# Kernel tuning notes

Hardware: AMD Instinct MI355X
Metric: run time of the kernel (lower is better)

## Reference

```python
import jax, jax.numpy as jnp
import numpy as np

B, H, W = 8, 64, 64
D = 256          # in_dim == key_dim == value_dim
HEADS = 8
DK = D // HEADS  # per-head channels (key == value)
EPS = 1e-5


def _ln(x, g, b):
    m = jnp.mean(x, axis=-1, keepdims=True)
    v = jnp.var(x, axis=-1, keepdims=True)
    return (x - m) * jax.lax.rsqrt(v + EPS) * g + b


def setup_inputs() -> dict:
    key = jax.random.key(0)
    ks = jax.random.split(key, 8)
    return {
        "x1": jax.random.normal(ks[0], (B, H, W, 2 * D), jnp.float32),
        "x2": jax.random.normal(ks[1], (B, H, W, D), jnp.float32),
        "linear_w": jax.random.normal(ks[2], (2 * D, D), jnp.float32) * 0.02,
        "linear_b": jax.random.normal(ks[3], (D,), jnp.float32) * 0.02,
        "ln1_g": jnp.ones((D,), jnp.float32) + jax.random.normal(ks[4], (D,), jnp.float32) * 0.02,
        "ln1_b": jax.random.normal(ks[5], (D,), jnp.float32) * 0.02,
        "reproj_w": jax.random.normal(ks[6], (2 * D, D), jnp.float32) * 0.02,  # 1x1 conv kernel [out,in]
        "reproj_b": jax.random.normal(ks[7], (2 * D,), jnp.float32) * 0.02,
        "ln_attn_g": jnp.ones((2 * D,), jnp.float32),
        "ln_attn_b": jnp.zeros((2 * D,), jnp.float32),
    }


def _cross_attention(n1, n2, reproj_w, reproj_b, ln_g, ln_b):
    # n1 (values source), n2 (keys/queries source): [B,H,W,D]
    N = H * W
    v = n1.reshape(B, N, D).transpose(0, 2, 1).reshape(B, HEADS, DK, N)
    kq = n2.reshape(B, N, D).transpose(0, 2, 1).reshape(B, HEADS, DK, N)
    k = jax.nn.softmax(kq, axis=-1)  # softmax over tokens (dim=2 in torch slice)
    q = jax.nn.softmax(kq, axis=2)   # softmax over per-head channels (dim=1 in torch slice)
    # attended[b,h,d,n] = sum_m sum_e q[b,h,d,m] k[b,h,e,m] v[b,h,e,n]
    ctx = jnp.einsum('bhdm,bhem->bhde', q, k)          # [B,h,dk,dk]
    att = jnp.einsum('bhde,bhen->bhdn', ctx, v)        # [B,h,dk,N]
    agg = att.reshape(B, D, H, W)                      # concat heads along channels
    rep = jnp.einsum('od,bdhw->bohw', reproj_w, agg) + reproj_b[None, :, None, None]
    rep = rep.transpose(0, 2, 3, 1)                    # [B,H,W,2D]
    return _ln(rep, ln_g, ln_b)


def reference(x1, x2, linear_w, linear_b, ln1_g, ln1_b, reproj_w, reproj_b, ln_attn_g, ln_attn_b):
    n1 = _ln(x1 @ linear_w + linear_b, ln1_g, ln1_b)   # [B,H,W,D]
    n2 = _ln(x2, ln1_g, ln1_b)                          # [B,H,W,D]
    attn = _cross_attention(n1, n2, reproj_w, reproj_b, ln_attn_g, ln_attn_b)
    return x1 + attn
```

## Files before the change

### kernel.cpp

```cpp
#include <hip/hip_runtime.h>
#include <stdint.h>

typedef __bf16 bf16x8 __attribute__((ext_vector_type(8)));
typedef float f32x4 __attribute__((ext_vector_type(4)));

#define EPS 1e-5f

__device__ __forceinline__ float b2f(unsigned short u) {
    union { unsigned int i; float f; } c; c.i = ((unsigned int)u) << 16; return c.f;
}
__device__ __forceinline__ unsigned short f2b(float f) {
    union { float f; unsigned int i; } c; c.f = f;
    unsigned int i = c.i;
    return (unsigned short)((i + 0x7FFFu + ((i >> 16) & 1u)) >> 16);
}

__global__ void k_zero(float* __restrict__ p, int n) {
    int i = blockIdx.x * 256 + threadIdx.x;
    if (i < n) p[i] = 0.0f;
}

__global__ void k_params(const float* __restrict__ lw, const float* __restrict__ rw,
                         const float* __restrict__ lb, const float* __restrict__ g1,
                         const float* __restrict__ b1, const float* __restrict__ rb,
                         const float* __restrict__ ga, const float* __restrict__ ba,
                         unsigned short* __restrict__ wt1,
                         unsigned short* __restrict__ rwb,
                         unsigned short* __restrict__ vec) {
    int gid = blockIdx.x * 256 + threadIdx.x;
    if (gid < 131072) {
        int k = gid >> 8, n = gid & 255;
        wt1[n * 512 + k] = f2b(lw[gid]);
    } else if (gid < 262144) {
        int j = gid - 131072;
        rwb[j] = f2b(rw[j]);
    } else if (gid < 264448) {
        int j = gid - 262144;
        if (j < 256)       vec[j] = f2b(lb[j]);
        else if (j < 512)  vec[j] = f2b(g1[j - 256]);
        else if (j < 768)  vec[j] = f2b(b1[j - 512]);
        else if (j < 1280) vec[j] = f2b(rb[j - 768]);
        else if (j < 1792) vec[j] = f2b(ga[j - 1280]);
        else               vec[j] = f2b(ba[j - 1792]);
    }
}

__global__ __launch_bounds__(256) void k_stats(const float* __restrict__ x2,
                                               float2* __restrict__ stats) {
    int t = threadIdx.x, lane = t & 63, w = t >> 6;
    size_t row = (size_t)blockIdx.x * 4 + w;
    float4 f = *(const float4*)(x2 + row * 256 + lane * 4);
    float s = f.x + f.y + f.z + f.w;
    float q = f.x * f.x + f.y * f.y + f.z * f.z + f.w * f.w;
#pragma unroll
    for (int msk = 1; msk < 64; msk <<= 1) {
        s += __shfl_xor(s, msk, 64);
        q += __shfl_xor(q, msk, 64);
    }
    float mn = s * (1.0f / 256.0f);
    float rstd = rsqrtf(q * (1.0f / 256.0f) - mn * mn + EPS);
    if (lane == 0) stats[row] = make_float2(mn, rstd);
}

__global__ __launch_bounds__(256) void k_ctx(const float* __restrict__ x2,
                                             const float2* __restrict__ stats,
                                             const unsigned short* __restrict__ vec,
                                             float* __restrict__ ctxraw) {
    __shared__ float E[64 * 36];
    __shared__ float Q[64 * 36];
    __shared__ float gs[32], bs[32];
    int bh = blockIdx.x >> 3;
    int b = bh >> 3, h = bh & 7;
    int ch = blockIdx.x & 7;
    int t = threadIdx.x;
    if (t < 32) { gs[t] = b2f(vec[256 + h * 32 + t]); bs[t] = b2f(vec[512 + h * 32 + t]); }
    __syncthreads();
    int d = t >> 3, e0 = (t & 7) * 4;
    float a0 = 0.f, a1 = 0.f, a2 = 0.f, a3 = 0.f;
    const float* base = x2 + ((size_t)b * 4096 + ch * 512) * 256 + h * 32;
    int srow = b * 4096 + ch * 512;
    const int m = t >> 2, c0 = (t & 3) * 8;
    for (int s0 = 0; s0 < 512; s0 += 64) {
        float2 st = stats[srow + s0 + m];
        const float4* p = (const float4*)(base + (size_t)(s0 + m) * 256 + c0);
        float4 f0 = p[0], f1 = p[1];
        float ev[8];
        ev[0] = __expf((f0.x - st.x) * st.y * gs[c0 + 0] + bs[c0 + 0]);
        ev[1] = __expf((f0.y - st.x) * st.y * gs[c0 + 1] + bs[c0 + 1]);
        ev[2] = __expf((f0.z - st.x) * st.y * gs[c0 + 2] + bs[c0 + 2]);
        ev[3] = __expf((f0.w - st.x) * st.y * gs[c0 + 3] + bs[c0 + 3]);
        ev[4] = __expf((f1.x - st.x) * st.y * gs[c0 + 4] + bs[c0 + 4]);
        ev[5] = __expf((f1.y - st.x) * st.y * gs[c0 + 5] + bs[c0 + 5]);
        ev[6] = __expf((f1.z - st.x) * st.y * gs[c0 + 6] + bs[c0 + 6]);
        ev[7] = __expf((f1.w - st.x) * st.y * gs[c0 + 7] + bs[c0 + 7]);
        float ps = ev[0] + ev[1] + ev[2] + ev[3] + ev[4] + ev[5] + ev[6] + ev[7];
        ps += __shfl_xor(ps, 1, 64);
        ps += __shfl_xor(ps, 2, 64);
        float qi = 1.0f / ps;
        *(float4*)(E + m * 36 + c0)     = make_float4(ev[0], ev[1], ev[2], ev[3]);
        *(float4*)(E + m * 36 + c0 + 4) = make_float4(ev[4], ev[5], ev[6], ev[7]);
        *(float4*)(Q + m * 36 + c0)     = make_float4(ev[0]*qi, ev[1]*qi, ev[2]*qi, ev[3]*qi);
        *(float4*)(Q + m * 36 + c0 + 4) = make_float4(ev[4]*qi, ev[5]*qi, ev[6]*qi, ev[7]*qi);
        __syncthreads();
#pragma unroll 4
        for (int mm = 0; mm < 64; mm++) {
            float qd = Q[mm * 36 + d];
            float4 e4 = *(const float4*)(E + mm * 36 + e0);
            a0 += qd * e4.x; a1 += qd * e4.y; a2 += qd * e4.z; a3 += qd * e4.w;
        }
        __syncthreads();
    }
    float* dst = ctxraw + ((size_t)bh << 10) + (d << 5) + e0;
    atomicAdd(dst + 0, a0);
    atomicAdd(dst + 1, a1);
    atomicAdd(dst + 2, a2);
    atomicAdd(dst + 3, a3);
}

__global__ __launch_bounds__(256) void k_w2(const float* __restrict__ ctxraw,
                                            const unsigned short* __restrict__ rwb,
                                            unsigned short* __restrict__ w2t) {
    __shared__ float ctx_s[1024];
    __shared__ float cinv[32];
    int blk = blockIdx.x;
    int b = blk >> 6, h = (blk >> 3) & 7, os = blk & 7;
    int bh = b * 8 + h;
    int t = threadIdx.x;
#pragma unroll
    for (int i = 0; i < 4; i++) ctx_s[t + 256 * i] = ctxraw[((size_t)bh << 10) + t + 256 * i];
    __syncthreads();
    if (t < 32) {
        float s = 0.f;
#pragma unroll
        for (int d = 0; d < 32; d++) s += ctx_s[d * 32 + t];
        cinv[t] = 1.0f / s;
    }
    __syncthreads();
    int o = os * 64 + (t >> 2);
    int e0 = (t & 3) * 8;
    float wv[32];
    const uint4* wp = (const uint4*)(rwb + (size_t)o * 256 + h * 32);
#pragma unroll
    for (int qd = 0; qd < 4; qd++) {
        uint4 u = wp[qd];
        unsigned int uu[4] = {u.x, u.y, u.z, u.w};
#pragma unroll
        for (int j = 0; j < 4; j++) {
            wv[qd * 8 + j * 2]     = b2f((unsigned short)(uu[j] & 0xFFFFu));
            wv[qd * 8 + j * 2 + 1] = b2f((unsigned short)(uu[j] >> 16));
        }
    }
    float s[8];
#pragma unroll
    for (int j = 0; j < 8; j++) s[j] = 0.f;
#pragma unroll 8
    for (int d = 0; d < 32; d++) {
        float w = wv[d];
#pragma unroll
        for (int j = 0; j < 8; j++) s[j] += ctx_s[d * 32 + e0 + j] * w;
    }
    ushort4 o4a, o4b;
    o4a.x = f2b(s[0] * cinv[e0 + 0]); o4a.y = f2b(s[1] * cinv[e0 + 1]);
    o4a.z = f2b(s[2] * cinv[e0 + 2]); o4a.w = f2b(s[3] * cinv[e0 + 3]);
    o4b.x = f2b(s[4] * cinv[e0 + 4]); o4b.y = f2b(s[5] * cinv[e0 + 5]);
    o4b.z = f2b(s[6] * cinv[e0 + 6]); o4b.w = f2b(s[7] * cinv[e0 + 7]);
    unsigned short* dst = w2t + ((size_t)b * 512 + o) * 256 + h * 32 + e0;
    *(ushort4*)dst = o4a;
    *(ushort4*)(dst + 4) = o4b;
}

__global__ __launch_bounds__(256) void k_gemm1(
    const float* __restrict__ x1, const unsigned short* __restrict__ wt1,
    const unsigned short* __restrict__ vec, unsigned short* __restrict__ n1) {
    __shared__ unsigned short pool[16896];
    unsigned short* As = pool;
    unsigned short* Bs = pool + 2560;
    unsigned short* n1s = pool;
    const int t = threadIdx.x;
    const int lane = t & 63, w = t >> 6;
    const int l15 = lane & 15, quad = lane >> 4;
    const int row0 = blockIdx.x * 64;
    const int mrow = (w << 4) + l15;
    const int k8 = quad * 8;
    const int stg_m = t >> 2, stg_k = (t & 3) * 8;

    f32x4 acc[16];
#pragma unroll
    for (int i = 0; i < 16; i++) acc[i] = (f32x4){0.f, 0.f, 0.f, 0.f};

    for (int k0 = 0; k0 < 512; k0 += 32) {
        {
            const float* xf = x1 + (size_t)(row0 + stg_m) * 512 + k0 + stg_k;
            float4 f0 = *(const float4*)xf;
            float4 f1 = *(const float4*)(xf + 4);
            ushort4 lo, hi;
            lo.x = f2b(f0.x); lo.y = f2b(f0.y); lo.z = f2b(f0.z); lo.w = f2b(f0.w);
            hi.x = f2b(f1.x); hi.y = f2b(f1.y); hi.z = f2b(f1.z); hi.w = f2b(f1.w);
            *(ushort4*)(As + stg_m * 40 + stg_k) = lo;
            *(ushort4*)(As + stg_m * 40 + stg_k + 4) = hi;
        }
#pragma unroll
        for (int p = 0; p < 4; p++) {
            int n = stg_m + p * 64;
            *(uint4*)(Bs + n * 40 + stg_k) =
                *(const uint4*)(wt1 + (size_t)n * 512 + k0 + stg_k);
        }
        __syncthreads();
        bf16x8 a = *(const bf16x8*)(As + mrow * 40 + k8);
#pragma unroll
        for (int cb = 0; cb < 16; cb++) {
            bf16x8 bf = *(const bf16x8*)(Bs + ((cb << 4) + l15) * 40 + k8);
            acc[cb] = __builtin_amdgcn_mfma_f32_16x16x32_bf16(a, bf, acc[cb], 0, 0, 0);
        }
        __syncthreads();
    }
#pragma unroll
    for (int cb = 0; cb < 16; cb++) {
        float bc = b2f(vec[(cb << 4) + l15]);
#pragma unroll
        for (int r = 0; r < 4; r++) acc[cb][r] += bc;
    }
    float mean_[4], rstd_[4];
#pragma unroll
    for (int r = 0; r < 4; r++) {
        float s = 0.f, q = 0.f;
#pragma unroll
        for (int cb = 0; cb < 16; cb++) { float v = acc[cb][r]; s += v; q += v * v; }
#pragma unroll
        for (int msk = 1; msk < 16; msk <<= 1) {
            s += __shfl_xor(s, msk, 64);
            q += __shfl_xor(q, msk, 64);
        }
        float mn = s * (1.0f / 256.0f);
        mean_[r] = mn;
        rstd_[r] = rsqrtf(q * (1.0f / 256.0f) - mn * mn + EPS);
    }
#pragma unroll
    for (int cb = 0; cb < 16; cb++) {
        int col = (cb << 4) + l15;
        float gg = b2f(vec[256 + col]), bbv = b2f(vec[512 + col]);
#pragma unroll
        for (int r = 0; r < 4; r++) {
            int rr = (w << 4) + (quad << 2) + r;
            n1s[rr * 264 + col] = f2b((acc[cb][r] - mean_[r]) * rstd_[r] * gg + bbv);
        }
    }
    __syncthreads();
    {
        int row = t >> 2;
        unsigned short* dst = n1 + (size_t)(row0 + row) * 256;
        const unsigned short* src = n1s + row * 264;
#pragma unroll
        for (int j = 0; j < 8; j++) {
            int chunk = (t & 3) * 8 + j;
            *(uint4*)(dst + chunk * 8) = *(const uint4*)(src + chunk * 8);
        }
    }
}

__global__ __launch_bounds__(512) void k_gemm2(
    const unsigned short* __restrict__ n1, const unsigned short* __restrict__ w2t,
    const unsigned short* __restrict__ vec, const float* __restrict__ x1,
    float* __restrict__ out) {
    __shared__ unsigned short As[64 * 40];
    __shared__ unsigned short Bs[512 * 40];
    __shared__ float2 red[2][64];
    const int t = threadIdx.x;
    const int lane = t & 63, w = t >> 6;
    const int l15 = lane & 15, quad = lane >> 4;
    const int hf = w >> 2, wr = w & 3;
    const int row0 = blockIdx.x * 64;
    const unsigned short* wb = w2t + (size_t)(row0 >> 12) * (512 * 256);
    const int mrow = (wr << 4) + l15;
    const int k8 = quad * 8;

    f32x4 acc[16];
#pragma unroll
    for (int i = 0; i < 16; i++) acc[i] = (f32x4){0.f, 0.f, 0.f, 0.f};

    for (int k0 = 0; k0 < 256; k0 += 32) {
        if (t < 256) {
            int m = t >> 2, kc = (t & 3) * 8;
            *(uint4*)(As + m * 40 + kc) =
                *(const uint4*)(n1 + (size_t)(row0 + m) * 256 + k0 + kc);
        }
#pragma unroll
        for (int p = 0; p < 4; p++) {
            int n = (t >> 2) + p * 128, kc = (t & 3) * 8;
            *(uint4*)(Bs + n * 40 + kc) =
                *(const uint4*)(wb + (size_t)n * 256 + k0 + kc);
        }
        __syncthreads();
        bf16x8 a = *(const bf16x8*)(As + mrow * 40 + k8);
#pragma unroll
        for (int cb = 0; cb < 16; cb++) {
            int ncol = (hf << 8) + (cb << 4) + l15;
            bf16x8 bf = *(const bf16x8*)(Bs + ncol * 40 + k8);
            acc[cb] = __builtin_amdgcn_mfma_f32_16x16x32_bf16(a, bf, acc[cb], 0, 0, 0);
        }
        __syncthreads();
    }
#pragma unroll
    for (int cb = 0; cb < 16; cb++) {
        float bc = b2f(vec[768 + (hf << 8) + (cb << 4) + l15]);
#pragma unroll
        for (int r = 0; r < 4; r++) acc[cb][r] += bc;
    }
#pragma unroll
    for (int r = 0; r < 4; r++) {
        float s = 0.f, q = 0.f;
#pragma unroll
        for (int cb = 0; cb < 16; cb++) { float v = acc[cb][r]; s += v; q += v * v; }
#pragma unroll
        for (int msk = 1; msk < 16; msk <<= 1) {
            s += __shfl_xor(s, msk, 64);
            q += __shfl_xor(q, msk, 64);
        }
        if (l15 == 0) red[hf][(wr << 4) + (quad << 2) + r] = make_float2(s, q);
    }
    __syncthreads();
    float mean_[4], rstd_[4];
#pragma unroll
    for (int r = 0; r < 4; r++) {
        int rl = (wr << 4) + (quad << 2) + r;
        float2 cA = red[0][rl], cB = red[1][rl];
        float s = cA.x + cB.x, q = cA.y + cB.y;
        float mn = s * (1.0f / 512.0f);
        mean_[r] = mn;
        rstd_[r] = rsqrtf(q * (1.0f / 512.0f) - mn * mn + EPS);
    }
#pragma unroll
    for (int cb = 0; cb < 16; cb++) {
        int col = (hf << 8) + (cb << 4) + l15;
        float gg = b2f(vec[1280 + col]), bbv = b2f(vec[1792 + col]);
#pragma unroll
        for (int r = 0; r < 4; r++) {
            size_t idx = (size_t)(row0 + (wr << 4) + (quad << 2) + r) * 512 + col;
            out[idx] = (acc[cb][r] - mean_[r]) * rstd_[r] * gg + bbv + x1[idx];
        }
    }
}

extern "C" void kernel_launch(void* const* d_in, const int* in_sizes, int n_in,
                              void* d_out, int out_size, void* d_ws, size_t ws_size,
                              hipStream_t stream) {
    const float* x1 = (const float*)d_in[0];
    const float* x2 = (const float*)d_in[1];
    const float* lw = (const float*)d_in[2];
    const float* lb = (const float*)d_in[3];
    const float* g1 = (const float*)d_in[4];
    const float* b1 = (const float*)d_in[5];
    const float* rw = (const float*)d_in[6];
    const float* rb = (const float*)d_in[7];
    const float* ga = (const float*)d_in[8];
    const float* ba = (const float*)d_in[9];
    float* out = (float*)d_out;

    char* ws = (char*)d_ws;
    float*          ctxr  = (float*)(ws);
    float2*         stats = (float2*)(ws + 262144);
    unsigned short* wt1   = (unsigned short*)(ws + 524288);
    unsigned short* rwb   = (unsigned short*)(ws + 786432);
    unsigned short* vec   = (unsigned short*)(ws + 1048576);
    unsigned short* w2t   = (unsigned short*)(ws + 1064960);
    unsigned short* n1    = (unsigned short*)(ws + 4194304);

    k_zero<<<dim3(256), dim3(256), 0, stream>>>(ctxr, 65536);
    k_params<<<dim3(1033), dim3(256), 0, stream>>>(lw, rw, lb, g1, b1, rb, ga, ba,
                                                   wt1, rwb, vec);
    k_stats<<<dim3(8192), dim3(256), 0, stream>>>(x2, stats);
    k_ctx<<<dim3(512), dim3(256), 0, stream>>>(x2, stats, vec, ctxr);
    k_w2<<<dim3(512), dim3(256), 0, stream>>>(ctxr, rwb, w2t);
    k_gemm1<<<dim3(512), dim3(256), 0, stream>>>(x1, wt1, vec, n1);
    k_gemm2<<<dim3(512), dim3(512), 0, stream>>>(n1, w2t, vec, x1, out);
}
```

Before: 244.7 us.

## Pre-tile GEMM weights and double-buffer them via direct global-to-LDS loads

```diff
diff --git a/kernel.cpp b/kernel.cpp
--- a/kernel.cpp
+++ b/kernel.cpp
@@ -5,6 +5,15 @@
 typedef float f32x4 __attribute__((ext_vector_type(4)));
 
 #define EPS 1e-5f
+
+#define WAITVM(N) asm volatile("s_waitcnt vmcnt(" #N ")" ::: "memory")
+#define WAITLGKM0 asm volatile("s_waitcnt lgkmcnt(0)" ::: "memory")
+
+__device__ __forceinline__ void gl16(const void* g, void* l) {
+    __builtin_amdgcn_global_load_lds(
+        (const __attribute__((address_space(1))) unsigned int*)g,
+        (__attribute__((address_space(3))) unsigned int*)l, 16, 0, 0);
+}
 
 __device__ __forceinline__ float b2f(unsigned short u) {
     union { unsigned int i; float f; } c; c.i = ((unsigned int)u) << 16; return c.f;
@@ -30,7 +39,7 @@
     int gid = blockIdx.x * 256 + threadIdx.x;
     if (gid < 131072) {
         int k = gid >> 8, n = gid & 255;
-        wt1[n * 512 + k] = f2b(lw[gid]);
+        wt1[((size_t)(k >> 3) * 256 + n) * 8 + (k & 7)] = f2b(lw[gid]);
     } else if (gid < 262144) {
         int j = gid - 131072;
         rwb[j] = f2b(rw[j]);
@@ -164,7 +173,8 @@
     o4a.z = f2b(s[2] * cinv[e0 + 2]); o4a.w = f2b(s[3] * cinv[e0 + 3]);
     o4b.x = f2b(s[4] * cinv[e0 + 4]); o4b.y = f2b(s[5] * cinv[e0 + 5]);
     o4b.z = f2b(s[6] * cinv[e0 + 6]); o4b.w = f2b(s[7] * cinv[e0 + 7]);
-    unsigned short* dst = w2t + ((size_t)b * 512 + o) * 256 + h * 32 + e0;
+    int kb = h * 4 + (e0 >> 3);
+    unsigned short* dst = w2t + (size_t)b * 131072 + ((size_t)kb * 512 + o) * 8;
     *(ushort4*)dst = o4a;
     *(ushort4*)(dst + 4) = o4b;
 }
@@ -172,47 +182,55 @@
 __global__ __launch_bounds__(256) void k_gemm1(
     const float* __restrict__ x1, const unsigned short* __restrict__ wt1,
     const unsigned short* __restrict__ vec, unsigned short* __restrict__ n1) {
-    __shared__ unsigned short pool[16896];
-    unsigned short* As = pool;
-    unsigned short* Bs = pool + 2560;
-    unsigned short* n1s = pool;
+    __shared__ __align__(16) char pool[33792];
     const int t = threadIdx.x;
     const int lane = t & 63, w = t >> 6;
     const int l15 = lane & 15, quad = lane >> 4;
-    const int row0 = blockIdx.x * 64;
+    const int rb = blockIdx.x;
+    const int row0 = rb * 64;
     const int mrow = (w << 4) + l15;
-    const int k8 = quad * 8;
-    const int stg_m = t >> 2, stg_k = (t & 3) * 8;
+
+    const float* xrow = x1 + (size_t)(row0 + mrow) * 512 + quad * 8;
 
     f32x4 acc[16];
 #pragma unroll
     for (int i = 0; i < 16; i++) acc[i] = (f32x4){0.f, 0.f, 0.f, 0.f};
 
-    for (int k0 = 0; k0 < 512; k0 += 32) {
-        {
-            const float* xf = x1 + (size_t)(row0 + stg_m) * 512 + k0 + stg_k;
-            float4 f0 = *(const float4*)xf;
-            float4 f1 = *(const float4*)(xf + 4);
-            ushort4 lo, hi;
-            lo.x = f2b(f0.x); lo.y = f2b(f0.y); lo.z = f2b(f0.z); lo.w = f2b(f0.w);
-            hi.x = f2b(f1.x); hi.y = f2b(f1.y); hi.z = f2b(f1.z); hi.w = f2b(f1.w);
-            *(ushort4*)(As + stg_m * 40 + stg_k) = lo;
-            *(ushort4*)(As + stg_m * 40 + stg_k + 4) = hi;
-        }
-#pragma unroll
-        for (int p = 0; p < 4; p++) {
-            int n = stg_m + p * 64;
-            *(uint4*)(Bs + n * 40 + stg_k) =
-                *(const uint4*)(wt1 + (size_t)n * 512 + k0 + stg_k);
-        }
-        __syncthreads();
-        bf16x8 a = *(const bf16x8*)(As + mrow * 40 + k8);
+    float4 fa[2][2];
+    fa[0][0] = *(const float4*)(xrow);
+    fa[0][1] = *(const float4*)(xrow + 4);
+#pragma unroll
+    for (int i = 0; i < 4; i++)
+        gl16((const char*)wt1 + (w * 4 + i) * 1024 + lane * 16,
+             pool + (w * 4 + i) * 1024);
+
+#pragma unroll
+    for (int s = 0; s < 16; ++s) {
+        const int cur = s & 1;
+        if (s < 15) {
+            const float* xn = xrow + (s + 1) * 32;
+            fa[cur ^ 1][0] = *(const float4*)xn;
+            fa[cur ^ 1][1] = *(const float4*)(xn + 4);
+#pragma unroll
+            for (int i = 0; i < 4; i++)
+                gl16((const char*)wt1 + (size_t)(s + 1) * 16384 + (w * 4 + i) * 1024 + lane * 16,
+                     pool + (cur ^ 1) * 16384 + (w * 4 + i) * 1024);
+        }
+        bf16x8 af;
+        af[0] = (__bf16)fa[cur][0].x; af[1] = (__bf16)fa[cur][0].y;
+        af[2] = (__bf16)fa[cur][0].z; af[3] = (__bf16)fa[cur][0].w;
+        af[4] = (__bf16)fa[cur][1].x; af[5] = (__bf16)fa[cur][1].y;
+        af[6] = (__bf16)fa[cur][1].z; af[7] = (__bf16)fa[cur][1].w;
+        if (s < 15) { WAITVM(6); } else { WAITVM(0); }
+        __builtin_amdgcn_s_barrier();
+        const char* Bc = pool + cur * 16384 + quad * 4096 + l15 * 16;
 #pragma unroll
         for (int cb = 0; cb < 16; cb++) {
-            bf16x8 bf = *(const bf16x8*)(Bs + ((cb << 4) + l15) * 40 + k8);
-            acc[cb] = __builtin_amdgcn_mfma_f32_16x16x32_bf16(a, bf, acc[cb], 0, 0, 0);
-        }
-        __syncthreads();
+            bf16x8 bf = *(const bf16x8*)(Bc + cb * 256);
+            acc[cb] = __builtin_amdgcn_mfma_f32_16x16x32_bf16(af, bf, acc[cb], 0, 0, 0);
+        }
+        WAITLGKM0;
+        __builtin_amdgcn_s_barrier();
     }
 #pragma unroll
     for (int cb = 0; cb < 16; cb++) {
@@ -235,6 +253,7 @@
         mean_[r] = mn;
         rstd_[r] = rsqrtf(q * (1.0f / 256.0f) - mn * mn + EPS);
     }
+    unsigned short* n1s = (unsigned short*)pool;
 #pragma unroll
     for (int cb = 0; cb < 16; cb++) {
         int col = (cb << 4) + l15;
@@ -245,15 +264,16 @@
             n1s[rr * 264 + col] = f2b((acc[cb][r] - mean_[r]) * rstd_[r] * gg + bbv);
         }
     }
-    __syncthreads();
+    WAITLGKM0;
+    __builtin_amdgcn_s_barrier();
     {
-        int row = t >> 2;
-        unsigned short* dst = n1 + (size_t)(row0 + row) * 256;
-        const unsigned short* src = n1s + row * 264;
+        int r = t >> 2;
+        const unsigned short* src = n1s + r * 264;
+        unsigned short* dst = n1 + (size_t)rb * 16384 + r * 8;
 #pragma unroll
         for (int j = 0; j < 8; j++) {
             int chunk = (t & 3) * 8 + j;
-            *(uint4*)(dst + chunk * 8) = *(const uint4*)(src + chunk * 8);
+            *(uint4*)(dst + chunk * 512) = *(const uint4*)(src + chunk * 8);
         }
     }
 }
@@ -262,43 +282,49 @@
     const unsigned short* __restrict__ n1, const unsigned short* __restrict__ w2t,
     const unsigned short* __restrict__ vec, const float* __restrict__ x1,
     float* __restrict__ out) {
-    __shared__ unsigned short As[64 * 40];
-    __shared__ unsigned short Bs[512 * 40];
-    __shared__ float2 red[2][64];
+    __shared__ __align__(16) char pool[66560];
+    __shared__ float2 red2[128];
     const int t = threadIdx.x;
     const int lane = t & 63, w = t >> 6;
     const int l15 = lane & 15, quad = lane >> 4;
     const int hf = w >> 2, wr = w & 3;
-    const int row0 = blockIdx.x * 64;
-    const unsigned short* wb = w2t + (size_t)(row0 >> 12) * (512 * 256);
-    const int mrow = (wr << 4) + l15;
-    const int k8 = quad * 8;
+    const int rb = blockIdx.x;
+    const int row0 = rb * 64;
+    const char* wb = (const char*)w2t + (size_t)(rb >> 6) * 262144;
+    const char* an = (const char*)n1 + (size_t)rb * 32768 + quad * 1024 + ((wr << 4) + l15) * 16;
 
     f32x4 acc[16];
 #pragma unroll
     for (int i = 0; i < 16; i++) acc[i] = (f32x4){0.f, 0.f, 0.f, 0.f};
 
-    for (int k0 = 0; k0 < 256; k0 += 32) {
-        if (t < 256) {
-            int m = t >> 2, kc = (t & 3) * 8;
-            *(uint4*)(As + m * 40 + kc) =
-                *(const uint4*)(n1 + (size_t)(row0 + m) * 256 + k0 + kc);
-        }
-#pragma unroll
-        for (int p = 0; p < 4; p++) {
-            int n = (t >> 2) + p * 128, kc = (t & 3) * 8;
-            *(uint4*)(Bs + n * 40 + kc) =
-                *(const uint4*)(wb + (size_t)n * 256 + k0 + kc);
-        }
-        __syncthreads();
-        bf16x8 a = *(const bf16x8*)(As + mrow * 40 + k8);
+    bf16x8 areg[2];
+    areg[0] = *(const bf16x8*)(an);
+#pragma unroll
+    for (int i = 0; i < 4; i++)
+        gl16(wb + (w * 4 + i) * 1024 + lane * 16, pool + (w * 4 + i) * 1024);
+
+#pragma unroll
+    for (int s = 0; s < 8; ++s) {
+        const int cur = s & 1;
+        if (s < 7) {
+            areg[cur ^ 1] = *(const bf16x8*)(an + (s + 1) * 4096);
+#pragma unroll
+            for (int i = 0; i < 4; i++)
+                gl16(wb + (size_t)(s + 1) * 32768 + (w * 4 + i) * 1024 + lane * 16,
+                     pool + (cur ^ 1) * 32768 + (w * 4 + i) * 1024);
+            WAITVM(5);
+        } else {
+            WAITVM(0);
+        }
+        __builtin_amdgcn_s_barrier();
+        const char* Bc = pool + cur * 32768 + quad * 8192 + hf * 4096 + l15 * 16;
 #pragma unroll
         for (int cb = 0; cb < 16; cb++) {
-            int ncol = (hf << 8) + (cb << 4) + l15;
-            bf16x8 bf = *(const bf16x8*)(Bs + ncol * 40 + k8);
-            acc[cb] = __builtin_amdgcn_mfma_f32_16x16x32_bf16(a, bf, acc[cb], 0, 0, 0);
-        }
-        __syncthreads();
+            bf16x8 bf = *(const bf16x8*)(Bc + cb * 256);
+            acc[cb] = __builtin_amdgcn_mfma_f32_16x16x32_bf16(areg[cur], bf, acc[cb], 0, 0, 0);
+        }
+        WAITLGKM0;
+        __builtin_amdgcn_s_barrier();
     }
 #pragma unroll
     for (int cb = 0; cb < 16; cb++) {
@@ -316,28 +342,54 @@
             s += __shfl_xor(s, msk, 64);
             q += __shfl_xor(q, msk, 64);
         }
-        if (l15 == 0) red[hf][(wr << 4) + (quad << 2) + r] = make_float2(s, q);
-    }
-    __syncthreads();
+        if (l15 == 0) red2[hf * 64 + (wr << 4) + (quad << 2) + r] = make_float2(s, q);
+    }
+    WAITLGKM0;
+    __builtin_amdgcn_s_barrier();
     float mean_[4], rstd_[4];
 #pragma unroll
     for (int r = 0; r < 4; r++) {
         int rl = (wr << 4) + (quad << 2) + r;
-        float2 cA = red[0][rl], cB = red[1][rl];
+        float2 cA = red2[rl], cB = red2[64 + rl];
         float s = cA.x + cB.x, q = cA.y + cB.y;
         float mn = s * (1.0f / 512.0f);
         mean_[r] = mn;
         rstd_[r] = rsqrtf(q * (1.0f / 512.0f) - mn * mn + EPS);
     }
-#pragma unroll
-    for (int cb = 0; cb < 16; cb++) {
-        int col = (hf << 8) + (cb << 4) + l15;
-        float gg = b2f(vec[1280 + col]), bbv = b2f(vec[1792 + col]);
-#pragma unroll
-        for (int r = 0; r < 4; r++) {
-            size_t idx = (size_t)(row0 + (wr << 4) + (quad << 2) + r) * 512 + col;
-            out[idx] = (acc[cb][r] - mean_[r]) * rstd_[r] * gg + bbv + x1[idx];
-        }
+    float* rep = (float*)pool;
+#pragma unroll
+    for (int hv = 0; hv < 2; ++hv) {
+        if (hv) __builtin_amdgcn_s_barrier();
+        if (hf == hv) {
+#pragma unroll
+            for (int cb = 0; cb < 16; cb++) {
+                int col = (cb << 4) + l15;
+                int gcol = (hv << 8) + col;
+                float gg = b2f(vec[1280 + gcol]), bbv = b2f(vec[1792 + gcol]);
+#pragma unroll
+                for (int r = 0; r < 4; r++)
+                    rep[((wr << 4) + (quad << 2) + r) * 260 + col] =
+                        (acc[cb][r] - mean_[r]) * rstd_[r] * gg + bbv;
+            }
+        }
+        WAITLGKM0;
+        __builtin_amdgcn_s_barrier();
+        int rr = t >> 4, c0 = (t & 15) << 2;
+#pragma unroll
+        for (int j = 0; j < 4; j++) {
+            int col = c0 + (j << 6);
+            float4 v0 = *(const float4*)(rep + rr * 260 + col);
+            float4 v1 = *(const float4*)(rep + (rr + 32) * 260 + col);
+            size_t g0 = (size_t)(row0 + rr) * 512 + (hv << 8) + col;
+            size_t g1 = g0 + (size_t)32 * 512;
+            float4 xa = *(const float4*)(x1 + g0);
+            float4 xb = *(const float4*)(x1 + g1);
+            v0.x += xa.x; v0.y += xa.y; v0.z += xa.z; v0.w += xa.w;
+            v1.x += xb.x; v1.y += xb.y; v1.z += xb.z; v1.w += xb.w;
+            *(float4*)(out + g0) = v0;
+            *(float4*)(out + g1) = v1;
+        }
+        WAITLGKM0;
     }
 }
 
```

New measurement: 234.6 us. -4.1%, faster.
